# Kernel tuning notes

Hardware: AMD Instinct MI355X
Metric: run time of the kernel (lower is better)

Reference implementation:

```python
import jax, jax.numpy as jnp
import numpy as np

DIM = 64
NUM_FEAT = 14
NUM_OUT = 105
N_NODES = 8192
N_EDGES = 16384
N_GRAPHS = 256
N_STEMS = 2048
N_JBONDS = 1024


def lrelu(v):
    return jax.nn.leaky_relu(v, 0.01)


def setup_inputs() -> dict:
    key = jax.random.key(0)
    ks = jax.random.split(key, 40)
    def rn(k, shape, s=0.1):
        return jax.random.normal(k, shape, dtype=jnp.float32) * s
    inp = {}
    inp['x'] = jax.random.normal(ks[0], (N_NODES, NUM_FEAT), dtype=jnp.float32)
    inp['edge_attr'] = jax.random.uniform(ks[1], (N_EDGES, 4), dtype=jnp.float32)
    inp['edge_index'] = jax.random.randint(ks[2], (2, N_EDGES), 0, N_NODES)
    inp['batch'] = jnp.sort(jax.random.randint(ks[3], (N_NODES,), 0, N_GRAPHS))
    inp['stem_atmidx'] = jax.random.randint(ks[4], (N_STEMS,), 0, N_NODES)
    inp['jbond_atmidx'] = jax.random.randint(ks[5], (N_JBONDS, 2), 0, N_NODES)
    # lin0
    inp['lin0_w'] = rn(ks[6], (NUM_FEAT, DIM)); inp['lin0_b'] = rn(ks[7], (DIM,))
    # NNConv edge net: Linear(4,dim) -> LeakyReLU -> Linear(dim, dim*dim)
    inp['net_w1'] = rn(ks[8], (4, DIM)); inp['net_b1'] = rn(ks[9], (DIM,))
    inp['net_w2'] = rn(ks[10], (DIM, DIM * DIM), 0.02); inp['net_b2'] = rn(ks[11], (DIM * DIM,), 0.02)
    # NNConv root weight + bias
    inp['conv_root'] = rn(ks[12], (DIM, DIM)); inp['conv_bias'] = rn(ks[13], (DIM,))
    # GRU (torch gate order r,z,n); stored [in, 3*dim]
    inp['gru_w_ih'] = rn(ks[14], (DIM, 3 * DIM)); inp['gru_w_hh'] = rn(ks[15], (DIM, 3 * DIM))
    inp['gru_b_ih'] = rn(ks[16], (3 * DIM,)); inp['gru_b_hh'] = rn(ks[17], (3 * DIM,))
    # node2stem MLP
    inp['n2s_w1'] = rn(ks[18], (DIM, DIM)); inp['n2s_b1'] = rn(ks[19], (DIM,))
    inp['n2s_w2'] = rn(ks[20], (DIM, NUM_OUT)); inp['n2s_b2'] = rn(ks[21], (NUM_OUT,))
    # node2jbond MLP
    inp['n2j_w1'] = rn(ks[22], (DIM, DIM)); inp['n2j_b1'] = rn(ks[23], (DIM,))
    inp['n2j_w2'] = rn(ks[24], (DIM, 1)); inp['n2j_b2'] = rn(ks[25], (1,))
    # Set2Set LSTM(2*dim -> dim), torch gate order i,f,g,o; stored [in, 4*dim]
    inp['s2s_w_ih'] = rn(ks[26], (2 * DIM, 4 * DIM)); inp['s2s_w_hh'] = rn(ks[27], (DIM, 4 * DIM))
    inp['s2s_b_ih'] = rn(ks[28], (4 * DIM,)); inp['s2s_b_hh'] = rn(ks[29], (4 * DIM,))
    # lin_out
    inp['lin_out_w'] = rn(ks[30], (2 * DIM, 2)); inp['lin_out_b'] = rn(ks[31], (2,))
    return inp


def reference(x, edge_attr, lin0_w, lin0_b, net_w1, net_b1, net_w2, net_b2,
              conv_root, conv_bias, gru_w_ih, gru_w_hh, gru_b_ih, gru_b_hh,
              n2s_w1, n2s_b1, n2s_w2, n2s_b2, n2j_w1, n2j_b1, n2j_w2, n2j_b2,
              s2s_w_ih, s2s_w_hh, s2s_b_ih, s2s_b_hh, lin_out_w, lin_out_b,
              edge_index, batch, stem_atmidx, jbond_atmidx):
    N = x.shape[0]
    src, dst = edge_index[0], edge_index[1]
    out = lrelu(x @ lin0_w + lin0_b)          # [N, dim]
    h = out
    # edge-conditioned weights (edge_attr is constant across the 6 iterations)
    ew = (lrelu(edge_attr @ net_w1 + net_b1) @ net_w2 + net_b2).reshape(-1, DIM, DIM)  # [E,dim,dim]
    deg = jnp.maximum(jax.ops.segment_sum(jnp.ones_like(dst, dtype=x.dtype), dst, num_segments=N), 1.0)[:, None]
    for _ in range(6):
        msg = jnp.einsum('ei,eio->eo', out[src], ew)                        # per-edge matmul
        agg = jax.ops.segment_sum(msg, dst, num_segments=N) / deg          # scatter-mean
        m = lrelu(agg + out @ conv_root + conv_bias)
        # GRU update (torch gate order r,z,n)
        gi = m @ gru_w_ih + gru_b_ih
        gh = h @ gru_w_hh + gru_b_hh
        ir, iz, inn = jnp.split(gi, 3, axis=-1)
        hr, hz, hn = jnp.split(gh, 3, axis=-1)
        r = jax.nn.sigmoid(ir + hr)
        z = jax.nn.sigmoid(iz + hz)
        n = jnp.tanh(inn + r * hn)
        h = (1.0 - z) * n + z * h
        out = h
    # per-stem block logits
    stem_preds = lrelu(out[stem_atmidx] @ n2s_w1 + n2s_b1) @ n2s_w2 + n2s_b2  # [S, num_out]
    # jbond: gather both endpoints, predict scalar, mean over the pair
    jb = out[jbond_atmidx.reshape(-1)]
    jpred = lrelu(jb @ n2j_w1 + n2j_b1) @ n2j_w2 + n2j_b2                     # [2J,1]
    jbond_preds = jpred.reshape(jbond_atmidx.shape).mean(axis=1)              # [J]
    # Set2Set, processing_steps=1
    B = N_GRAPHS
    hS = jnp.zeros((B, DIM), x.dtype)
    cS = jnp.zeros((B, DIM), x.dtype)
    q_star = jnp.zeros((B, 2 * DIM), x.dtype)
    gates = q_star @ s2s_w_ih + s2s_b_ih + hS @ s2s_w_hh + s2s_b_hh
    gi_, gf_, gg_, go_ = jnp.split(gates, 4, axis=-1)
    cS = jax.nn.sigmoid(gf_) * cS + jax.nn.sigmoid(gi_) * jnp.tanh(gg_)
    hS = jax.nn.sigmoid(go_) * jnp.tanh(cS)
    q = hS                                                                    # [B, dim]
    e = jnp.sum(out * q[batch], axis=-1)                                      # [N]
    emax = jax.ops.segment_max(e, batch, num_segments=B)
    a_un = jnp.exp(e - emax[batch])
    a = a_un / jax.ops.segment_sum(a_un, batch, num_segments=B)[batch]
    r_pool = jax.ops.segment_sum(a[:, None] * out, batch, num_segments=B)     # [B, dim]
    q_star = jnp.concatenate([q, r_pool], axis=1)                             # [B, 2*dim]
    scalar_outs = q_star @ lin_out_w + lin_out_b                              # [B, 2]
    return (scalar_outs, stem_preds, jbond_preds)
```

## Files before the change

### kernel.cpp

```cpp
#include <hip/hip_runtime.h>

#define DIM 64
#define NF 14
#define NOUT 105
#define NN 8192
#define NE 16384
#define NB 256
#define NS 2048
#define NJ 1024
#define KTOT 4160
#define KSPLIT 8

#define C_X      0
#define C_EA     114688
#define C_L0W    180224
#define C_L0B    181120
#define C_NW1    181184
#define C_NB1    181440
#define C_NW2    181504
#define C_NB2    443648
#define C_CRT    447744
#define C_CB     451840
#define C_GWIH   451904
#define C_GWHH   464192
#define C_GBIH   476480
#define C_GBHH   476672
#define C_SW1    476864
#define C_SB1    480960
#define C_SW2    481024
#define C_SB2    487744
#define C_JW1    487856
#define C_JB1    491952
#define C_JW2    492016
#define C_JB2    492080
#define C_S2IH   492088
#define C_S2HH   492344
#define C_LOW    492600
#define C_LOB    492856
#define C_TOT    492864

typedef float f32x4 __attribute__((ext_vector_type(4)));
typedef short bf16x8 __attribute__((ext_vector_type(8)));

__device__ __forceinline__ float bf2f(unsigned short u){
  union { unsigned int i; float f; } v; v.i = ((unsigned int)u) << 16; return v.f;
}
__device__ __forceinline__ unsigned short f2bf(float f){
  union { float f; unsigned int i; } v; v.f = f;
  unsigned int x = v.i;
  return (unsigned short)((x + 0x7FFFu + ((x >> 16) & 1u)) >> 16);
}
__device__ __forceinline__ float sigm(float x){ return 1.f / (1.f + __expf(-x)); }
__device__ __forceinline__ float tanh_f(float x){
  x = fminf(10.f, fmaxf(-10.f, x));
  float e = __expf(2.f * x);
  return (e - 1.f) / (e + 1.f);
}
__device__ __forceinline__ float lrelu(float x){ return x > 0.f ? x : 0.01f * x; }

__device__ __forceinline__ float wred_sum(float v){
  #pragma unroll
  for (int off = 32; off > 0; off >>= 1) v += __shfl_xor(v, off, 64);
  return v;
}
__device__ __forceinline__ float wred_max(float v){
  #pragma unroll
  for (int off = 32; off > 0; off >>= 1) v = fmaxf(v, __shfl_xor(v, off, 64));
  return v;
}


__global__ void k_detect(const unsigned short* __restrict__ ea, int* __restrict__ flag){
  __shared__ int cnt;
  if (threadIdx.x == 0) cnt = 0;
  __syncthreads();
  int c = 0;
  for (int i = threadIdx.x; i < 8192; i += 256) c += (ea[2*i] >> 15) & 1;
  atomicAdd(&cnt, c);
  __syncthreads();
  if (threadIdx.x == 0) *flag = (cnt > 100) ? 1 : 0;
}

struct CvtArgs {
  const void* src[26];
  int n[26];
  int off[26];
};

__global__ void k_cvt(CvtArgs a, const int* __restrict__ flag, unsigned short* __restrict__ dst){
  bool f32 = (*flag != 0);
  int gid = blockIdx.x * blockDim.x + threadIdx.x, gs = gridDim.x * blockDim.x;
  #pragma unroll 1
  for (int j = 0; j < 26; ++j){
    const void* s = a.src[j];
    int n = a.n[j], o = a.off[j];
    for (int i = gid; i < n; i += gs)
      dst[o + i] = f32 ? f2bf(((const float*)s)[i]) : ((const unsigned short*)s)[i];
  }
}


__global__ void k_deg(const int* __restrict__ ei, float* __restrict__ deg){
  int e = blockIdx.x * blockDim.x + threadIdx.x;
  if (e < NE) atomicAdd(&deg[ei[NE + e]], 1.0f);
}

__global__ void k_lin0(const unsigned short* __restrict__ cvt,
                       float* __restrict__ actF, unsigned short* __restrict__ actB){
  const unsigned short* x = cvt + C_X;
  const unsigned short* w = cvt + C_L0W;
  const unsigned short* b = cvt + C_L0B;
  int idx = blockIdx.x * blockDim.x + threadIdx.x;
  int n = idx >> 6, d = idx & 63;
  float acc = bf2f(b[d]);
  #pragma unroll
  for (int f = 0; f < NF; ++f) acc += bf2f(x[n*NF + f]) * bf2f(w[f*DIM + d]);
  float v = lrelu(acc);
  actF[idx] = v; actB[idx] = f2bf(v);
}

__global__ void k_u(const unsigned short* __restrict__ cvt, unsigned short* __restrict__ u){
  const unsigned short* ea = cvt + C_EA;
  const unsigned short* w  = cvt + C_NW1;
  const unsigned short* b  = cvt + C_NB1;
  int idx = blockIdx.x * blockDim.x + threadIdx.x;
  int e = idx >> 6, d = idx & 63;
  float acc = bf2f(b[d]);
  #pragma unroll
  for (int f = 0; f < 4; ++f) acc += bf2f(ea[e*4 + f]) * bf2f(w[f*DIM + d]);
  u[idx] = f2bf(lrelu(acc));
}

__global__ void k_w2t(const unsigned short* __restrict__ cvt, unsigned short* __restrict__ w2t){
  const unsigned short* w2 = cvt + C_NW2;
  int t = blockIdx.x * blockDim.x + threadIdx.x;
  int n = t >> 6, k = t & 63;
  w2t[t] = w2[k*4096 + (n & 63)*64 + (n >> 6)];
}

__global__ void k_w2r(const unsigned short* __restrict__ cvt, unsigned short* __restrict__ w2rt){
  const unsigned short* w2 = cvt + C_NW2;
  const unsigned short* b2 = cvt + C_NB2;
  int t = blockIdx.x * blockDim.x + threadIdx.x;
  int o = t / KTOT, k = t - o * KTOT;
  unsigned short v = (k < 4096) ? w2[(k >> 6) * 4096 + (k & 63) * 64 + o]
                                : b2[(k - 4096) * 64 + o];
  w2rt[t] = v;
}

__global__ void k_prep(const unsigned short* __restrict__ cvt,
                       unsigned short* __restrict__ crt, unsigned short* __restrict__ btg,
                       float* __restrict__ cbg, float* __restrict__ qv){
  const unsigned short* cr  = cvt + C_CRT;
  const unsigned short* wih = cvt + C_GWIH;
  const unsigned short* whh = cvt + C_GWHH;
  const unsigned short* bih = cvt + C_GBIH;
  const unsigned short* bhh = cvt + C_GBHH;
  const unsigned short* s2sbih = cvt + C_S2IH;
  const unsigned short* s2sbhh = cvt + C_S2HH;
  int tid = threadIdx.x;
  for (int t = tid; t < 4096; t += 256){ int n = t & 63, k = t >> 6; crt[n*64 + k] = cr[k*64 + n]; }
  for (int t = tid; t < 32768; t += 256){
    int nidx = t >> 7, kidx = t & 127;
    int g = nidx >> 6, d = nidx & 63, ki = kidx & 63;
    unsigned short v = 0;
    if (kidx < 64){
      if (g == 0) v = wih[ki*192 + d];
      else if (g == 1) v = wih[ki*192 + 64 + d];
      else if (g == 2) v = wih[ki*192 + 128 + d];
    } else {
      if (g == 0) v = whh[ki*192 + d];
      else if (g == 1) v = whh[ki*192 + 64 + d];
      else if (g == 3) v = whh[ki*192 + 128 + d];
    }
    btg[nidx*128 + kidx] = v;
  }
  if (tid < 256){
    int g = tid >> 6, d = tid & 63;
    float v;
    if (g == 0) v = bf2f(bih[d]) + bf2f(bhh[d]);
    else if (g == 1) v = bf2f(bih[64 + d]) + bf2f(bhh[64 + d]);
    else if (g == 2) v = bf2f(bih[128 + d]);
    else v = bf2f(bhh[128 + d]);
    cbg[tid] = v;
  }
  if (tid < 64){
    float gi = bf2f(s2sbih[tid])       + bf2f(s2sbhh[tid]);
    float gg = bf2f(s2sbih[128 + tid]) + bf2f(s2sbhh[128 + tid]);
    float go = bf2f(s2sbih[192 + tid]) + bf2f(s2sbhh[192 + tid]);
    float c = sigm(gi) * tanh_f(gg);
    qv[tid] = sigm(go) * tanh_f(c);
  }
}


__global__ __launch_bounds__(256) void k_ew(const unsigned short* __restrict__ z,
                                            const unsigned short* __restrict__ w2t,
                                            const unsigned short* __restrict__ cvt,
                                            unsigned short* __restrict__ ew){
  const unsigned short* b2 = cvt + C_NB2;
  __shared__ __align__(16) unsigned short tile[4][4096];
  int w = threadIdx.x >> 6, lane = threadIdx.x & 63;
  int lm = lane & 15, q8 = (lane >> 4) * 8, rq = (lane >> 4) * 4;
  int e0 = blockIdx.x * 64;
  int n0 = blockIdx.y * 256 + w * 64;
  f32x4 acc[4][4];
  #pragma unroll
  for (int mt = 0; mt < 4; ++mt)
    #pragma unroll
    for (int nt = 0; nt < 4; ++nt) acc[mt][nt] = (f32x4){0.f, 0.f, 0.f, 0.f};
  #pragma unroll
  for (int kk = 0; kk < 2; ++kk){
    bf16x8 af[4], bfr[4];
    #pragma unroll
    for (int mt = 0; mt < 4; ++mt)
      af[mt] = *(const bf16x8*)&z[(size_t)(e0 + mt*16 + lm)*64 + kk*32 + q8];
    #pragma unroll
    for (int nt = 0; nt < 4; ++nt)
      bfr[nt] = *(const bf16x8*)&w2t[(size_t)(n0 + nt*16 + lm)*64 + kk*32 + q8];
    #pragma unroll
    for (int mt = 0; mt < 4; ++mt)
      #pragma unroll
      for (int nt = 0; nt < 4; ++nt)
        acc[mt][nt] = __builtin_amdgcn_mfma_f32_16x16x32_bf16(af[mt], bfr[nt], acc[mt][nt], 0, 0, 0);
  }
  #pragma unroll
  for (int nt = 0; nt < 4; ++nt){
    int col = nt*16 + lm;
    int gcol = n0 + col;
    float bb = bf2f(b2[((gcol & 63) << 6) | (gcol >> 6)]);
    #pragma unroll
    for (int mt = 0; mt < 4; ++mt)
      #pragma unroll
      for (int r = 0; r < 4; ++r){
        int row = mt*16 + rq + r;
        int phys = (col >> 3) ^ (row & 7);
        tile[w][row*64 + phys*8 + (col & 7)] = f2bf(acc[mt][nt][r] + bb);
      }
  }
  #pragma unroll
  for (int it = 0; it < 8; ++it){
    int row = it*8 + (lane >> 3);
    int c16 = lane & 7;
    int phys = c16 ^ (row & 7);
    bf16x8 v = *(const bf16x8*)&tile[w][row*64 + phys*8];
    *(bf16x8*)&ew[(size_t)(e0 + row)*4096 + n0 + c16*8] = v;
  }
}

__global__ __launch_bounds__(256) void k_msg(const unsigned short* __restrict__ actB,
                                             const unsigned short* __restrict__ ew,
                                             const int* __restrict__ ei,
                                             float* __restrict__ agg){
  __shared__ __align__(16) float sact[4][64];
  int w = threadIdx.x >> 6, lane = threadIdx.x & 63;
  int e = blockIdx.x * 4 + w;
  int src = ei[e], dst = ei[NE + e];
  sact[w][lane] = bf2f(actB[(size_t)src*64 + lane]);
  __syncthreads();
  const unsigned short* ep = ew + (size_t)e*4096 + (size_t)lane*64;
  float acc = 0.f;
  #pragma unroll
  for (int t = 0; t < 8; ++t){
    bf16x8 v = *(const bf16x8*)(ep + t*8);
    f32x4 sa = *(const f32x4*)&sact[w][t*8];
    f32x4 sb = *(const f32x4*)&sact[w][t*8 + 4];
    acc += bf2f((unsigned short)v[0]) * sa[0];
    acc += bf2f((unsigned short)v[1]) * sa[1];
    acc += bf2f((unsigned short)v[2]) * sa[2];
    acc += bf2f((unsigned short)v[3]) * sa[3];
    acc += bf2f((unsigned short)v[4]) * sb[0];
    acc += bf2f((unsigned short)v[5]) * sb[1];
    acc += bf2f((unsigned short)v[6]) * sb[2];
    acc += bf2f((unsigned short)v[7]) * sb[3];
  }
  atomicAdd(&agg[(size_t)dst*64 + lane], acc);
}


__global__ __launch_bounds__(256) void k_msgf(const unsigned short* __restrict__ actB,
                                              const unsigned short* __restrict__ z,
                                              const unsigned short* __restrict__ w2rt,
                                              const int* __restrict__ ei,
                                              float* __restrict__ agg){
  __shared__ __align__(16) unsigned short sz[256 * 8];
  int w = threadIdx.x >> 6, lane = threadIdx.x & 63;
  int lm = lane & 15, q8 = (lane >> 4) * 8, rq = (lane >> 4) * 4;
  int e0 = blockIdx.x * 256;
  int s  = blockIdx.y;
  {
    int t = threadIdx.x;
    *(uint4*)&sz[t * 8] = *(const uint4*)&z[(size_t)(e0 + t) * 64 + s * 8];
  }
  __syncthreads();

  uint4 apack[4][2];
  #pragma unroll
  for (int mt = 0; mt < 4; ++mt){
    int src = ei[e0 + w*64 + mt*16 + lm];
    apack[mt][0] = *(const uint4*)&actB[(size_t)src * 64 + q8];
    apack[mt][1] = *(const uint4*)&actB[(size_t)src * 64 + 32 + q8];
  }

  f32x4 acc[4][4];
  #pragma unroll
  for (int mt = 0; mt < 4; ++mt)
    #pragma unroll
    for (int nt = 0; nt < 4; ++nt) acc[mt][nt] = (f32x4){0.f, 0.f, 0.f, 0.f};

  int kk0 = s * 16;
  int nk = (s == KSPLIT - 1) ? 18 : 16;
  for (int c = 0; c < nk; ++c){
    int kk = kk0 + c;
    bf16x8 bfr[4];
    #pragma unroll
    for (int nt = 0; nt < 4; ++nt)
      bfr[nt] = *(const bf16x8*)&w2rt[(size_t)(nt*16 + lm) * KTOT + kk*32 + q8];
    #pragma unroll
    for (int mt = 0; mt < 4; ++mt){
      float zf = 1.0f;
      if (kk < 128){
        int erow = w*64 + mt*16 + lm;
        zf = bf2f(sz[erow * 8 + ((kk >> 1) & 7)]);
      }
      uint4 ap = apack[mt][kk & 1];
      bf16x8 af;
      #pragma unroll
      for (int h = 0; h < 4; ++h){
        unsigned int dw = ((const unsigned int*)&ap)[h];
        float flo = __uint_as_float(dw << 16) * zf;
        float fhi = __uint_as_float(dw & 0xFFFF0000u) * zf;
        unsigned int pk = ((unsigned int)f2bf(flo)) | (((unsigned int)f2bf(fhi)) << 16);
        ((unsigned int*)&af)[h] = pk;
      }
      #pragma unroll
      for (int nt = 0; nt < 4; ++nt)
        acc[mt][nt] = __builtin_amdgcn_mfma_f32_16x16x32_bf16(af, bfr[nt], acc[mt][nt], 0, 0, 0);
    }
  }

  #pragma unroll
  for (int mt = 0; mt < 4; ++mt){
    int dstv[4];
    #pragma unroll
    for (int r = 0; r < 4; ++r) dstv[r] = ei[NE + e0 + w*64 + mt*16 + rq + r];
    #pragma unroll
    for (int nt = 0; nt < 4; ++nt)
      #pragma unroll
      for (int r = 0; r < 4; ++r)
        atomicAdd(&agg[(size_t)dstv[r] * 64 + nt*16 + lm], acc[mt][nt][r]);
  }
}


__global__ __launch_bounds__(256) void k_gru(const unsigned short* __restrict__ actB_in,
                                             const float* __restrict__ actF_in,
                                             float* __restrict__ agg, const float* __restrict__ deg,
                                             const unsigned short* __restrict__ crt,
                                             const unsigned short* __restrict__ cvt,
                                             const unsigned short* __restrict__ btg,
                                             const float* __restrict__ cbg,
                                             float* __restrict__ actF_out, unsigned short* __restrict__ actB_out){
  const unsigned short* cbias = cvt + C_CB;
  __shared__ __align__(16) unsigned short s_frag[2*4*16*8];
  int w = threadIdx.x >> 6, lane = threadIdx.x & 63;
  int lm = lane & 15, q = lane >> 4;
  int q8 = q*8, rq = q*4;
  int r0 = blockIdx.x * 16;
  f32x4 am = (f32x4){0.f, 0.f, 0.f, 0.f};
  #pragma unroll
  for (int kk = 0; kk < 2; ++kk){
    bf16x8 a = *(const bf16x8*)&actB_in[(size_t)(r0 + lm)*64 + kk*32 + q8];
    bf16x8 b = *(const bf16x8*)&crt[(size_t)(w*16 + lm)*64 + kk*32 + q8];
    am = __builtin_amdgcn_mfma_f32_16x16x32_bf16(a, b, am, 0, 0, 0);
  }
  {
    int col = w*16 + lm;
    float cb = bf2f(cbias[col]);
    int kk2 = w >> 1, q2 = (w & 1)*2 + (lm >> 3), j = lm & 7;
    #pragma unroll
    for (int r = 0; r < 4; ++r){
      int row = r0 + rq + r;
      float dg = fmaxf(deg[row], 1.f);
      float v = am[r] + agg[(size_t)row*64 + col] / dg + cb;
      agg[(size_t)row*64 + col] = 0.f;
      s_frag[((kk2*4 + q2)*16 + (rq + r))*8 + j] = f2bf(lrelu(v));
    }
  }
  __syncthreads();
  f32x4 g[4];
  #pragma unroll
  for (int t = 0; t < 4; ++t) g[t] = (f32x4){0.f, 0.f, 0.f, 0.f};
  #pragma unroll
  for (int kk = 0; kk < 4; ++kk){
    bf16x8 a;
    if (kk < 2) a = *(const bf16x8*)&s_frag[(kk*4 + q)*128 + lm*8];
    else        a = *(const bf16x8*)&actB_in[(size_t)(r0 + lm)*64 + (kk - 2)*32 + q8];
    #pragma unroll
    for (int t = 0; t < 4; ++t){
      bf16x8 b = *(const bf16x8*)&btg[(size_t)(t*64 + w*16 + lm)*128 + kk*32 + q8];
      g[t] = __builtin_amdgcn_mfma_f32_16x16x32_bf16(a, b, g[t], 0, 0, 0);
    }
  }
  {
    int d = w*16 + lm;
    float cb_r = cbg[d], cb_z = cbg[64 + d], cb_n = cbg[128 + d], cb_h = cbg[192 + d];
    #pragma unroll
    for (int r = 0; r < 4; ++r){
      int row = r0 + rq + r;
      float rr = sigm(g[0][r] + cb_r);
      float zz = sigm(g[1][r] + cb_z);
      float nn = tanh_f(g[2][r] + cb_n + rr * (g[3][r] + cb_h));
      float ho = actF_in[(size_t)row*64 + d];
      float hn2 = (1.f - zz) * nn + zz * ho;
      actF_out[(size_t)row*64 + d] = hn2;
      actB_out[(size_t)row*64 + d] = f2bf(hn2);
    }
  }
}


__device__ __forceinline__ int lower_bound_batch(const int* b, int val){
  int lo = 0, hi = NN;
  while (lo < hi){ int mid = (lo + hi) >> 1; if (b[mid] < val) lo = mid + 1; else hi = mid; }
  return lo;
}

__device__ __forceinline__ void store_out(void* outp, const int* flag, size_t idx, float v){
  if (*flag) ((float*)outp)[idx] = v;
  else       ((unsigned short*)outp)[idx] = f2bf(v);
}

__global__ __launch_bounds__(64) void k_graph(const float* __restrict__ act,
                                              const int* __restrict__ batch, const float* __restrict__ qv,
                                              const unsigned short* __restrict__ cvt,
                                              const int* __restrict__ flag,
                                              void* __restrict__ outp){
  const unsigned short* lw = cvt + C_LOW;
  const unsigned short* lb = cvt + C_LOB;
  __shared__ float se[512];
  int b = blockIdx.x, lane = threadIdx.x;
  int lo = lower_bound_batch(batch, b);
  int hi = lower_bound_batch(batch, b + 1);
  int cnt = hi - lo; if (cnt > 512) cnt = 512;
  float qvl = qv[lane];
  for (int ii = 0; ii < cnt; ++ii){
    float p = act[(size_t)(lo + ii)*64 + lane] * qvl;
    p = wred_sum(p);
    if (lane == 0) se[ii] = p;
  }
  __syncthreads();
  float em = -3.4e38f;
  for (int ii = lane; ii < cnt; ii += 64) em = fmaxf(em, se[ii]);
  em = wred_max(em);
  float sm = 0.f;
  for (int ii = lane; ii < cnt; ii += 64) sm += __expf(se[ii] - em);
  float denom = wred_sum(sm);
  float rp = 0.f;
  for (int ii = 0; ii < cnt; ++ii) rp += __expf(se[ii] - em) * act[(size_t)(lo + ii)*64 + lane];
  if (cnt > 0 && denom > 0.f) rp /= denom;
  float s0 = qvl*bf2f(lw[lane*2])     + rp*bf2f(lw[(64 + lane)*2]);
  float s1 = qvl*bf2f(lw[lane*2 + 1]) + rp*bf2f(lw[(64 + lane)*2 + 1]);
  s0 = wred_sum(s0); s1 = wred_sum(s1);
  if (lane == 0){
    store_out(outp, flag, b*2,     s0 + bf2f(lb[0]));
    store_out(outp, flag, b*2 + 1, s1 + bf2f(lb[1]));
  }
}

__global__ __launch_bounds__(256) void k_stem(const float* __restrict__ act, const int* __restrict__ sidx,
                                              const unsigned short* __restrict__ cvt,
                                              const int* __restrict__ flag,
                                              void* __restrict__ outp){
  const unsigned short* w1 = cvt + C_SW1;
  const unsigned short* b1 = cvt + C_SB1;
  const unsigned short* w2 = cvt + C_SW2;
  const unsigned short* b2 = cvt + C_SB2;
  __shared__ float sa[4][64], st[4][64];
  int w = threadIdx.x >> 6, lane = threadIdx.x & 63;
  int s = blockIdx.x * 4 + w;
  int a = sidx[s];
  sa[w][lane] = act[(size_t)a*64 + lane];
  __syncthreads();
  float t = bf2f(b1[lane]);
  #pragma unroll 8
  for (int i = 0; i < 64; ++i) t += sa[w][i] * bf2f(w1[i*64 + lane]);
  st[w][lane] = lrelu(t);
  __syncthreads();
  size_t base = 512 + (size_t)s * NOUT;
  float v = bf2f(b2[lane]);
  #pragma unroll 8
  for (int d = 0; d < 64; ++d) v += st[w][d] * bf2f(w2[d*NOUT + lane]);
  store_out(outp, flag, base + lane, v);
  int o2 = 64 + lane;
  if (o2 < NOUT){
    float v2 = bf2f(b2[o2]);
    #pragma unroll 8
    for (int d = 0; d < 64; ++d) v2 += st[w][d] * bf2f(w2[d*NOUT + o2]);
    store_out(outp, flag, base + o2, v2);
  }
}

__global__ __launch_bounds__(256) void k_jbond(const float* __restrict__ act, const int* __restrict__ jidx,
                                               const unsigned short* __restrict__ cvt,
                                               const int* __restrict__ flag,
                                               void* __restrict__ outp){
  const unsigned short* w1 = cvt + C_JW1;
  const unsigned short* b1 = cvt + C_JB1;
  const unsigned short* w2 = cvt + C_JW2;
  const unsigned short* b2 = cvt + C_JB2;
  __shared__ float a0[4][64], a1[4][64];
  int w = threadIdx.x >> 6, lane = threadIdx.x & 63;
  int j = blockIdx.x * 4 + w;
  int i0 = jidx[j*2], i1 = jidx[j*2 + 1];
  a0[w][lane] = act[(size_t)i0*64 + lane];
  a1[w][lane] = act[(size_t)i1*64 + lane];
  __syncthreads();
  float t0 = bf2f(b1[lane]), t1 = t0;
  #pragma unroll 8
  for (int i = 0; i < 64; ++i){
    float wv = bf2f(w1[i*64 + lane]);
    t0 += a0[w][i] * wv;
    t1 += a1[w][i] * wv;
  }
  t0 = lrelu(t0); t1 = lrelu(t1);
  float p = (t0 + t1) * bf2f(w2[lane]);
  p = wred_sum(p);
  if (lane == 0) store_out(outp, flag, 512 + (size_t)NS*NOUT + j, 0.5f * p + bf2f(b2[0]));
}


extern "C" void kernel_launch(void* const* d_in, const int* in_sizes, int n_in,
                              void* d_out, int out_size, void* d_ws, size_t ws_size,
                              hipStream_t stream){
  (void)in_sizes; (void)n_in; (void)out_size;
  const int* edge_index = (const int*)d_in[2];
  const int* batch      = (const int*)d_in[3];
  const int* stem_idx   = (const int*)d_in[4];
  const int* jbond_idx  = (const int*)d_in[5];

  char* ws = (char*)d_ws;
  size_t off = 0;
  auto alloc = [&](size_t bytes) -> void* {
    void* p = ws + off; off += (bytes + 255) & ~(size_t)255; return p;
  };
  unsigned short* cvt  = (unsigned short*)alloc((size_t)C_TOT * 2);
  unsigned short* w2t  = (unsigned short*)alloc((size_t)4096 * 64 * 2);
  unsigned short* w2rt = (unsigned short*)alloc((size_t)64 * KTOT * 2);
  unsigned short* z_bf = (unsigned short*)alloc((size_t)NE * 64 * 2);
  float* actF0 = (float*)alloc((size_t)NN * 64 * 4);
  float* actF1 = (float*)alloc((size_t)NN * 64 * 4);
  unsigned short* actB0 = (unsigned short*)alloc((size_t)NN * 64 * 2);
  unsigned short* actB1 = (unsigned short*)alloc((size_t)NN * 64 * 2);
  float* deg  = (float*)alloc(NN * 4);
  float* agg  = (float*)alloc((size_t)NN * 64 * 4);
  unsigned short* crt = (unsigned short*)alloc(64 * 64 * 2);
  unsigned short* btg = (unsigned short*)alloc(256 * 128 * 2);
  float* cbg  = (float*)alloc(256 * 4);
  float* qv   = (float*)alloc(64 * 4);
  int* flag   = (int*)alloc(256);
  size_t ew_bytes = (size_t)NE * 4096 * 2;
  bool big = (off + ew_bytes) <= ws_size;
  unsigned short* ew = big ? (unsigned short*)alloc(ew_bytes) : nullptr;

  hipMemsetAsync(deg, 0, ((size_t)NN * 4) + ((size_t)NN * 64 * 4) + 256, stream);

  k_detect<<<1, 256, 0, stream>>>((const unsigned short*)d_in[1], flag);

  CvtArgs ca;
  const int srcIdx[26] = {0,1,6,7,8,9,10,11,12,13,14,15,16,17,18,19,20,21,22,23,24,25,28,29,30,31};
  const int ns[26]  = {114688,65536,896,64,256,64,262144,4096,4096,64,12288,12288,192,192,
                       4096,64,6720,105,4096,64,64,1,256,256,256,2};
  const int ofs[26] = {C_X,C_EA,C_L0W,C_L0B,C_NW1,C_NB1,C_NW2,C_NB2,C_CRT,C_CB,C_GWIH,C_GWHH,
                       C_GBIH,C_GBHH,C_SW1,C_SB1,C_SW2,C_SB2,C_JW1,C_JB1,C_JW2,C_JB2,
                       C_S2IH,C_S2HH,C_LOW,C_LOB};
  for (int j = 0; j < 26; ++j){ ca.src[j] = d_in[srcIdx[j]]; ca.n[j] = ns[j]; ca.off[j] = ofs[j]; }
  k_cvt<<<512, 256, 0, stream>>>(ca, flag, cvt);

  k_deg<<<NE/256, 256, 0, stream>>>(edge_index, deg);
  k_lin0<<<NN*DIM/256, 256, 0, stream>>>(cvt, actF0, actB0);
  k_u<<<NE*DIM/256, 256, 0, stream>>>(cvt, z_bf);
  k_prep<<<1, 256, 0, stream>>>(cvt, crt, btg, cbg, qv);

  if (big){
    k_w2t<<<4096*64/256, 256, 0, stream>>>(cvt, w2t);
    k_ew<<<dim3(NE/64, 16), 256, 0, stream>>>(z_bf, w2t, cvt, ew);
  } else {
    k_w2r<<<64*KTOT/256, 256, 0, stream>>>(cvt, w2rt);
  }

  for (int t = 0; t < 6; ++t){
    const float* aF_in  = (t & 1) ? actF1 : actF0;
    float* aF_out       = (t & 1) ? actF0 : actF1;
    const unsigned short* aB_in = (t & 1) ? actB1 : actB0;
    unsigned short* aB_out      = (t & 1) ? actB0 : actB1;
    if (big)
      k_msg<<<NE/4, 256, 0, stream>>>(aB_in, ew, edge_index, agg);
    else
      k_msgf<<<dim3(NE/256, KSPLIT), 256, 0, stream>>>(aB_in, z_bf, w2rt, edge_index, agg);
    k_gru<<<NN/16, 256, 0, stream>>>(aB_in, aF_in, agg, deg, crt, cvt, btg, cbg,
                                     aF_out, aB_out);
  }
  k_graph<<<NB, 64, 0, stream>>>(actF0, batch, qv, cvt, flag, d_out);
  k_stem<<<NS/4, 256, 0, stream>>>(actF0, stem_idx, cvt, flag, d_out);
  k_jbond<<<NJ/4, 256, 0, stream>>>(actF0, jbond_idx, cvt, flag, d_out);
}
```

Baseline: 454.2 us.

## Replace atomic scatter aggregation with CSR-based per-node gather

Builds a CSR incoming-edge list once (scan of degrees plus atomic fill). The message kernel then writes per-edge bf16 messages, and a new gather kernel sums them per destination node without float atomics. The GRU kernel no longer zeroes agg, and the fallback path memsets agg each step. This adds an extra kernel launch and a msgv round trip per step, plus bf16 rounding of messages, in exchange for removing contended atomics.

```diff
diff --git a/kernel.cpp b/kernel.cpp
--- a/kernel.cpp
+++ b/kernel.cpp
@@ -9,7 +9,6 @@
 #define NS 2048
 #define NJ 1024
 #define KTOT 4160
-#define KSPLIT 8
 
 #define C_X      0
 #define C_EA     114688
@@ -105,6 +104,42 @@
   if (e < NE) atomicAdd(&deg[ei[NE + e]], 1.0f);
 }
 
+__global__ __launch_bounds__(256) void k_scan(const float* __restrict__ deg,
+                                              int* __restrict__ offsets, int* __restrict__ cursor){
+  __shared__ int part[256];
+  int t = threadIdx.x;
+  int s = 0;
+  #pragma unroll 4
+  for (int i = 0; i < 32; ++i) s += (int)deg[t*32 + i];
+  part[t] = s;
+  __syncthreads();
+  for (int d = 1; d < 256; d <<= 1){
+    int v = (t >= d) ? part[t - d] : 0;
+    __syncthreads();
+    part[t] += v;
+    __syncthreads();
+  }
+  int run = (t == 0) ? 0 : part[t - 1];
+  #pragma unroll 4
+  for (int i = 0; i < 32; ++i){
+    int n = t*32 + i;
+    offsets[n] = run;
+    cursor[n] = 0;
+    run += (int)deg[n];
+  }
+  if (t == 255) offsets[NN] = run;
+}
+
+__global__ void k_fill(const int* __restrict__ ei, const int* __restrict__ offsets,
+                       int* __restrict__ cursor, int* __restrict__ list){
+  int e = blockIdx.x * blockDim.x + threadIdx.x;
+  if (e < NE){
+    int dst = ei[NE + e];
+    int pos = atomicAdd(&cursor[dst], 1);
+    list[offsets[dst] + pos] = e;
+  }
+}
+
 __global__ void k_lin0(const unsigned short* __restrict__ cvt,
                        float* __restrict__ actF, unsigned short* __restrict__ actB){
   const unsigned short* x = cvt + C_X;
@@ -248,14 +283,14 @@
   }
 }
 
-__global__ __launch_bounds__(256) void k_msg(const unsigned short* __restrict__ actB,
-                                             const unsigned short* __restrict__ ew,
-                                             const int* __restrict__ ei,
-                                             float* __restrict__ agg){
+__global__ __launch_bounds__(256) void k_msgv(const unsigned short* __restrict__ actB,
+                                              const unsigned short* __restrict__ ew,
+                                              const int* __restrict__ ei,
+                                              unsigned short* __restrict__ msgv){
   __shared__ __align__(16) float sact[4][64];
   int w = threadIdx.x >> 6, lane = threadIdx.x & 63;
   int e = blockIdx.x * 4 + w;
-  int src = ei[e], dst = ei[NE + e];
+  int src = ei[e];
   sact[w][lane] = bf2f(actB[(size_t)src*64 + lane]);
   __syncthreads();
   const unsigned short* ep = ew + (size_t)e*4096 + (size_t)lane*64;
@@ -274,7 +309,22 @@
     acc += bf2f((unsigned short)v[6]) * sb[2];
     acc += bf2f((unsigned short)v[7]) * sb[3];
   }
-  atomicAdd(&agg[(size_t)dst*64 + lane], acc);
+  msgv[(size_t)e*64 + lane] = f2bf(acc);
+}
+
+__global__ __launch_bounds__(256) void k_agg(const unsigned short* __restrict__ msgv,
+                                             const int* __restrict__ offsets,
+                                             const int* __restrict__ list,
+                                             float* __restrict__ agg){
+  int w = threadIdx.x >> 6, lane = threadIdx.x & 63;
+  int v = blockIdx.x * 4 + w;
+  int ib = offsets[v], ie = offsets[v + 1];
+  float acc = 0.f;
+  for (int j = ib; j < ie; ++j){
+    int e = list[j];
+    acc += bf2f(msgv[(size_t)e*64 + lane]);
+  }
+  agg[(size_t)v*64 + lane] = acc;
 }
 
 
@@ -293,7 +343,6 @@
     *(uint4*)&sz[t * 8] = *(const uint4*)&z[(size_t)(e0 + t) * 64 + s * 8];
   }
   __syncthreads();
-
   uint4 apack[4][2];
   #pragma unroll
   for (int mt = 0; mt < 4; ++mt){
@@ -301,15 +350,13 @@
     apack[mt][0] = *(const uint4*)&actB[(size_t)src * 64 + q8];
     apack[mt][1] = *(const uint4*)&actB[(size_t)src * 64 + 32 + q8];
   }
-
   f32x4 acc[4][4];
   #pragma unroll
   for (int mt = 0; mt < 4; ++mt)
     #pragma unroll
     for (int nt = 0; nt < 4; ++nt) acc[mt][nt] = (f32x4){0.f, 0.f, 0.f, 0.f};
-
   int kk0 = s * 16;
-  int nk = (s == KSPLIT - 1) ? 18 : 16;
+  int nk = (s == 7) ? 18 : 16;
   for (int c = 0; c < nk; ++c){
     int kk = kk0 + c;
     bf16x8 bfr[4];
@@ -338,24 +385,22 @@
         acc[mt][nt] = __builtin_amdgcn_mfma_f32_16x16x32_bf16(af, bfr[nt], acc[mt][nt], 0, 0, 0);
     }
   }
-
   #pragma unroll
   for (int mt = 0; mt < 4; ++mt){
-    int dstv[4];
-    #pragma unroll
-    for (int r = 0; r < 4; ++r) dstv[r] = ei[NE + e0 + w*64 + mt*16 + rq + r];
-    #pragma unroll
-    for (int nt = 0; nt < 4; ++nt)
+    #pragma unroll
+    for (int r = 0; r < 4; ++r){
+      int dst = ei[NE + e0 + w*64 + mt*16 + rq + r];
       #pragma unroll
-      for (int r = 0; r < 4; ++r)
-        atomicAdd(&agg[(size_t)dstv[r] * 64 + nt*16 + lm], acc[mt][nt][r]);
+      for (int nt = 0; nt < 4; ++nt)
+        atomicAdd(&agg[(size_t)dst * 64 + nt*16 + lm], acc[mt][nt][r]);
+    }
   }
 }
 
 
 __global__ __launch_bounds__(256) void k_gru(const unsigned short* __restrict__ actB_in,
                                              const float* __restrict__ actF_in,
-                                             float* __restrict__ agg, const float* __restrict__ deg,
+                                             const float* __restrict__ agg, const float* __restrict__ deg,
                                              const unsigned short* __restrict__ crt,
                                              const unsigned short* __restrict__ cvt,
                                              const unsigned short* __restrict__ btg,
@@ -383,7 +428,6 @@
       int row = r0 + rq + r;
       float dg = fmaxf(deg[row], 1.f);
       float v = am[r] + agg[(size_t)row*64 + col] / dg + cb;
-      agg[(size_t)row*64 + col] = 0.f;
       s_frag[((kk2*4 + q2)*16 + (rq + r))*8 + j] = f2bf(lrelu(v));
     }
   }
@@ -548,6 +592,7 @@
   unsigned short* w2t  = (unsigned short*)alloc((size_t)4096 * 64 * 2);
   unsigned short* w2rt = (unsigned short*)alloc((size_t)64 * KTOT * 2);
   unsigned short* z_bf = (unsigned short*)alloc((size_t)NE * 64 * 2);
+  unsigned short* msgv = z_bf;
   float* actF0 = (float*)alloc((size_t)NN * 64 * 4);
   float* actF1 = (float*)alloc((size_t)NN * 64 * 4);
   unsigned short* actB0 = (unsigned short*)alloc((size_t)NN * 64 * 2);
@@ -559,11 +604,14 @@
   float* cbg  = (float*)alloc(256 * 4);
   float* qv   = (float*)alloc(64 * 4);
   int* flag   = (int*)alloc(256);
+  int* offsets = (int*)alloc((NN + 1) * 4);
+  int* cursor  = (int*)alloc(NN * 4);
+  int* list    = (int*)alloc(NE * 4);
   size_t ew_bytes = (size_t)NE * 4096 * 2;
   bool big = (off + ew_bytes) <= ws_size;
   unsigned short* ew = big ? (unsigned short*)alloc(ew_bytes) : nullptr;
 
-  hipMemsetAsync(deg, 0, ((size_t)NN * 4) + ((size_t)NN * 64 * 4) + 256, stream);
+  hipMemsetAsync(deg, 0, NN * sizeof(float), stream);
 
   k_detect<<<1, 256, 0, stream>>>((const unsigned short*)d_in[1], flag);
 
@@ -578,6 +626,8 @@
   k_cvt<<<512, 256, 0, stream>>>(ca, flag, cvt);
 
   k_deg<<<NE/256, 256, 0, stream>>>(edge_index, deg);
+  k_scan<<<1, 256, 0, stream>>>(deg, offsets, cursor);
+  k_fill<<<NE/256, 256, 0, stream>>>(edge_index, offsets, cursor, list);
   k_lin0<<<NN*DIM/256, 256, 0, stream>>>(cvt, actF0, actB0);
   k_u<<<NE*DIM/256, 256, 0, stream>>>(cvt, z_bf);
   k_prep<<<1, 256, 0, stream>>>(cvt, crt, btg, cbg, qv);
@@ -594,10 +644,13 @@
     float* aF_out       = (t & 1) ? actF0 : actF1;
     const unsigned short* aB_in = (t & 1) ? actB1 : actB0;
     unsigned short* aB_out      = (t & 1) ? actB0 : actB1;
-    if (big)
-      k_msg<<<NE/4, 256, 0, stream>>>(aB_in, ew, edge_index, agg);
-    else
-      k_msgf<<<dim3(NE/256, KSPLIT), 256, 0, stream>>>(aB_in, z_bf, w2rt, edge_index, agg);
+    if (big){
+      k_msgv<<<NE/4, 256, 0, stream>>>(aB_in, ew, edge_index, msgv);
+      k_agg<<<NN/4, 256, 0, stream>>>(msgv, offsets, list, agg);
+    } else {
+      hipMemsetAsync(agg, 0, (size_t)NN * 64 * sizeof(float), stream);
+      k_msgf<<<dim3(NE/256, 8), 256, 0, stream>>>(aB_in, z_bf, w2rt, edge_index, agg);
+    }
     k_gru<<<NN/16, 256, 0, stream>>>(aB_in, aF_in, agg, deg, crt, cvt, btg, cbg,
                                      aF_out, aB_out);
   }
```

Result: slower. 516.7 us (+13.8%).
